# Kernel optimization log

Hardware: AMD Instinct MI355X
Metric: run time of the kernel (lower is better)

## Reference

```python
import jax, jax.numpy as jnp
import numpy as np

EPS = 1e-5


def gcn_conv(x, W, b, src, dst, ew, num_nodes):
    """GCNConv with add_self_loops=True, symmetric normalization (PyG default)."""
    # degree at destination, self-loop weight 1.0 included implicitly
    deg = jax.ops.segment_sum(ew, dst, num_segments=num_nodes) + 1.0  # [N]
    dinv = jax.lax.rsqrt(deg)                                         # deg >= 1
    norm = dinv[src] * ew * dinv[dst]                                 # [E]
    h = x @ W                                                         # [N, F]
    msg = norm[:, None] * h[src]                                      # [E, F]
    agg = jax.ops.segment_sum(msg, dst, num_segments=num_nodes)       # [N, F]
    # self-loop contribution: dinv[i] * 1 * dinv[i] = 1/deg[i]
    agg = agg + h * (1.0 / deg)[:, None]
    return agg + b


def batchnorm(h, gamma, beta):
    mean = jnp.mean(h, axis=0)
    var = jnp.mean(jnp.square(h - mean), axis=0)  # biased, training-mode stats
    return (h - mean) * jax.lax.rsqrt(var + EPS) * gamma + beta


def setup_inputs() -> dict:
    key = jax.random.key(0)
    ks = jax.random.split(key, 8)
    N, E, F = 50000, 800000, 64
    x = jax.random.normal(ks[0], (N, F), dtype=jnp.float32)
    edge_index = jax.random.randint(ks[1], (2, E), 0, N, dtype=jnp.int64)
    edge_weight = jax.random.uniform(ks[2], (E,), dtype=jnp.float32)
    s = 1.0 / np.sqrt(F)
    W1 = jax.random.uniform(ks[3], (F, F), jnp.float32, -s, s)
    b1 = jnp.zeros((F,), jnp.float32)
    W2 = jax.random.uniform(ks[4], (F, F), jnp.float32, -s, s)
    b2 = jnp.zeros((F,), jnp.float32)
    gamma1 = jnp.ones((F,), jnp.float32)
    beta1 = jnp.zeros((F,), jnp.float32)
    gamma2 = jnp.ones((F,), jnp.float32)
    beta2 = jnp.zeros((F,), jnp.float32)
    return {"x": x, "edge_index": edge_index, "edge_weight": edge_weight,
            "W1": W1, "b1": b1, "gamma1": gamma1, "beta1": beta1,
            "W2": W2, "b2": b2, "gamma2": gamma2, "beta2": beta2}


def reference(x, edge_index, edge_weight, W1, b1, gamma1, beta1, W2, b2, gamma2, beta2):
    N = x.shape[0]
    src, dst = edge_index[0], edge_index[1]
    identity = x
    out = gcn_conv(x, W1, b1, src, dst, edge_weight, N)
    out = jax.nn.relu(batchnorm(out, gamma1, beta1))
    out = gcn_conv(out, W2, b2, src, dst, edge_weight, N)
    out = batchnorm(out, gamma2, beta2)
    out = out + identity  # residual: num_input_features == hidden_dim
    return jax.nn.relu(out)
```

## Files before the change

### kernel.cpp

```cpp
#include <hip/hip_runtime.h>
#include <math.h>

#define FEAT 64
#define BN_EPS 1e-5f
#define BN_REPS 64

__device__ __forceinline__ int edge_idx(const void* p, int is64, long long i) {
    return is64 ? (int)((const long long*)p)[i] : ((const int*)p)[i];
}

__device__ __forceinline__ float4 f4fma(float a, float4 b, float4 c) {
    return make_float4(fmaf(a, b.x, c.x), fmaf(a, b.y, c.y),
                       fmaf(a, b.z, c.z), fmaf(a, b.w, c.w));
}

__device__ __forceinline__ unsigned bf16rtne(float f) {
    unsigned u = __float_as_uint(f);
    return (u + 0x7fffu + ((u >> 16) & 1u)) >> 16;
}
__device__ __forceinline__ unsigned packbf2(float a, float b) {
    return bf16rtne(a) | (bf16rtne(b) << 16);
}
__device__ __forceinline__ float4 unpackbf4(uint2 r) {
    return make_float4(__uint_as_float(r.x << 16),
                       __uint_as_float(r.x & 0xffff0000u),
                       __uint_as_float(r.y << 16),
                       __uint_as_float(r.y & 0xffff0000u));
}

__global__ __launch_bounds__(256) void init_kernel(
    const unsigned* __restrict__ w, int* __restrict__ flag,
    int* __restrict__ cnt, float* __restrict__ parts, int N) {
    int i = blockIdx.x * 256 + threadIdx.x;
    if (i < N) cnt[i] = 0;
    if (blockIdx.x < 64) parts[blockIdx.x * 256 + threadIdx.x] = 0.0f;
    if (blockIdx.x == 0 && threadIdx.x < 64) {
        unsigned long long ok = __ballot(w[2 * threadIdx.x + 1] == 0u);
        if (threadIdx.x == 0) *flag = (ok == ~0ull);
    }
}

__global__ __launch_bounds__(256) void count_seq_kernel(
    const void* __restrict__ ei, const int* __restrict__ flag,
    int* __restrict__ cnt, int* __restrict__ seq, int E) {
    int is64 = *flag;
    int T = gridDim.x * 256;
    int i = blockIdx.x * 256 + threadIdx.x;
#pragma unroll
    for (int u = 0; u < 8; ++u) {
        int e = i + u * T;
        if (e < E) {
            int dst = edge_idx(ei, is64, (long long)E + e);
            seq[e] = atomicAdd(&cnt[dst], 1);
        }
    }
}

__global__ __launch_bounds__(256) void scan1_kernel(const int* __restrict__ cnt,
                                                    int* __restrict__ excl,
                                                    int* __restrict__ bsum, int N) {
    __shared__ int tmp[256];
    int i = blockIdx.x * 256 + threadIdx.x;
    int v = (i < N) ? cnt[i] : 0;
    tmp[threadIdx.x] = v;
    __syncthreads();
    for (int off = 1; off < 256; off <<= 1) {
        int t = (threadIdx.x >= off) ? tmp[threadIdx.x - off] : 0;
        __syncthreads();
        tmp[threadIdx.x] += t;
        __syncthreads();
    }
    if (i < N) excl[i] = tmp[threadIdx.x] - v;
    if (threadIdx.x == 255) bsum[blockIdx.x] = tmp[255];
}

__global__ __launch_bounds__(256) void scan2_kernel(int* __restrict__ bsum, int nb) {
    __shared__ int tmp[256];
    int i = threadIdx.x;
    int v = (i < nb) ? bsum[i] : 0;
    tmp[i] = v;
    __syncthreads();
    for (int off = 1; off < 256; off <<= 1) {
        int t = (i >= off) ? tmp[i - off] : 0;
        __syncthreads();
        tmp[i] += t;
        __syncthreads();
    }
    if (i < nb) bsum[i] = tmp[i] - v;
}

__global__ void scan3_kernel(const int* __restrict__ excl,
                             const int* __restrict__ bsum,
                             int* __restrict__ rowptr, int N, int E) {
    int i = blockIdx.x * 256 + threadIdx.x;
    if (i < N) rowptr[i] = excl[i] + bsum[blockIdx.x];
    if (i == 0) rowptr[N] = E;
}

__global__ __launch_bounds__(256) void scatter_csr_kernel(
    const void* __restrict__ ei, const float* __restrict__ ew,
    const int* __restrict__ flag, const int* __restrict__ rowptr,
    const int* __restrict__ seq, int2* __restrict__ csr, int E) {
    int is64 = *flag;
    int T = gridDim.x * 256;
    int i = blockIdx.x * 256 + threadIdx.x;
#pragma unroll
    for (int u = 0; u < 2; ++u) {
        int e = i + u * T;
        if (e < E) {
            int src = edge_idx(ei, is64, e);
            int dst = edge_idx(ei, is64, (long long)E + e);
            int pos = rowptr[dst] + seq[e];
            csr[pos] = make_int2(src, __float_as_int(ew[e]));
        }
    }
}

__global__ __launch_bounds__(256) void deg_inv_kernel(
    const int* __restrict__ rowptr, const int2* __restrict__ csr,
    float* __restrict__ dinv, float* __restrict__ invdeg, int N) {
    int t = blockIdx.x * 256 + threadIdx.x;
    int n = t >> 3, l = t & 7;
    if (n >= N) return;
    int b = rowptr[n], e = rowptr[n + 1];
    float d = 0.0f;
    for (int k = b + l; k < e; k += 8) d += __int_as_float(csr[k].y);
    d += __shfl_xor(d, 1);
    d += __shfl_xor(d, 2);
    d += __shfl_xor(d, 4);
    if (l == 0) {
        d += 1.0f;
        dinv[n]   = rsqrtf(d);
        invdeg[n] = 1.0f / d;
    }
}

__global__ __launch_bounds__(256) void fold_kernel(int2* __restrict__ csr,
                                                   const float* __restrict__ dinv,
                                                   int E) {
    int T = gridDim.x * 256;
    int i = blockIdx.x * 256 + threadIdx.x;
#pragma unroll
    for (int u = 0; u < 2; ++u) {
        int e = i + u * T;
        if (e < E) {
            int2 v = csr[e];
            csr[e].y = __float_as_int(dinv[v.x] * __int_as_float(v.y));
        }
    }
}

__global__ __launch_bounds__(256) void gemm64_kernel(
    const float* __restrict__ in, const float* __restrict__ W,
    const float* __restrict__ scale, const float* __restrict__ shift,
    uint2* __restrict__ out_bf, int N, int affine) {
    __shared__ float4 Ws4[64][16];
    __shared__ float xs[64][65];
    __shared__ float sA[64], sS[64];
    int tid = threadIdx.x;
    const float4* W4 = (const float4*)W;
    for (int j = tid; j < 1024; j += 256) Ws4[j >> 4][j & 15] = W4[j];
    if (affine && tid < 64) { sA[tid] = scale[tid]; sS[tid] = shift[tid]; }
    __syncthreads();

    int rowBase = blockIdx.x * 64;
    for (int j = tid; j < 1024; j += 256) {
        int r = j >> 4, q = j & 15;
        int row = rowBase + r;
        float4 v = make_float4(0.f, 0.f, 0.f, 0.f);
        if (row < N) {
            v = ((const float4*)in)[(size_t)row * 16 + q];
            if (affine) {
                int c = q * 4;
                v.x = fmaxf(fmaf(v.x, sA[c + 0], sS[c + 0]), 0.f);
                v.y = fmaxf(fmaf(v.y, sA[c + 1], sS[c + 1]), 0.f);
                v.z = fmaxf(fmaf(v.z, sA[c + 2], sS[c + 2]), 0.f);
                v.w = fmaxf(fmaf(v.w, sA[c + 3], sS[c + 3]), 0.f);
            }
        }
        xs[r][q * 4 + 0] = v.x;
        xs[r][q * 4 + 1] = v.y;
        xs[r][q * 4 + 2] = v.z;
        xs[r][q * 4 + 3] = v.w;
    }
    __syncthreads();

    int q = tid & 15, rg = tid >> 4;
    int r0 = rg * 4;
    float4 a0 = make_float4(0.f, 0.f, 0.f, 0.f), a1 = a0, a2 = a0, a3 = a0;
#pragma unroll 4
    for (int k = 0; k < 64; ++k) {
        float4 wv = Ws4[k][q];
        a0 = f4fma(xs[r0 + 0][k], wv, a0);
        a1 = f4fma(xs[r0 + 1][k], wv, a1);
        a2 = f4fma(xs[r0 + 2][k], wv, a2);
        a3 = f4fma(xs[r0 + 3][k], wv, a3);
    }
    int row = rowBase + r0;
    if (row + 0 < N) out_bf[(size_t)(row + 0) * 16 + q] = make_uint2(packbf2(a0.x, a0.y), packbf2(a0.z, a0.w));
    if (row + 1 < N) out_bf[(size_t)(row + 1) * 16 + q] = make_uint2(packbf2(a1.x, a1.y), packbf2(a1.z, a1.w));
    if (row + 2 < N) out_bf[(size_t)(row + 2) * 16 + q] = make_uint2(packbf2(a2.x, a2.y), packbf2(a2.z, a2.w));
    if (row + 3 < N) out_bf[(size_t)(row + 3) * 16 + q] = make_uint2(packbf2(a3.x, a3.y), packbf2(a3.z, a3.w));
}

__global__ __launch_bounds__(256) void gather_agg_kernel(
    const uint2* __restrict__ h2, const int* __restrict__ rowptr,
    const int2* __restrict__ csr, const float* __restrict__ dinv,
    const float* __restrict__ invdeg, const float* __restrict__ bias,
    float* __restrict__ agg, float* __restrict__ parts, int N) {
    int tid = threadIdx.x;
    int wave = tid >> 6, lane = tid & 63;
    int sub = lane >> 4, sl = lane & 15;
    float4 bv = ((const float4*)bias)[sl];
    float4 bnS = make_float4(0.f, 0.f, 0.f, 0.f), bnQ = bnS;

    int n = blockIdx.x * 4 + wave;
    if (n < N) {
        int beg = rowptr[n], end = rowptr[n + 1];
        uint2 selfr = h2[(size_t)n * 16 + sl];
        float dn = dinv[n], idg = invdeg[n];

        float4 accE = make_float4(0.f, 0.f, 0.f, 0.f);
        for (int k = beg; k < end; k += 16) {
            int srcs[4]; float w[4];
#pragma unroll
            for (int j = 0; j < 4; ++j) {
                int idx = k + sub + 4 * j;
                if (idx < end) {
                    int2 ed = csr[idx];
                    srcs[j] = ed.x; w[j] = __int_as_float(ed.y);
                } else { srcs[j] = 0; w[j] = 0.f; }
            }
            uint2 hr[4];
#pragma unroll
            for (int j = 0; j < 4; ++j)
                hr[j] = (k + sub + 4 * j < end)
                          ? h2[(size_t)srcs[j] * 16 + sl] : make_uint2(0u, 0u);
#pragma unroll
            for (int j = 0; j < 4; ++j)
                accE = f4fma(w[j], unpackbf4(hr[j]), accE);
        }
        accE.x += __shfl_xor(accE.x, 16); accE.y += __shfl_xor(accE.y, 16);
        accE.z += __shfl_xor(accE.z, 16); accE.w += __shfl_xor(accE.w, 16);
        accE.x += __shfl_xor(accE.x, 32); accE.y += __shfl_xor(accE.y, 32);
        accE.z += __shfl_xor(accE.z, 32); accE.w += __shfl_xor(accE.w, 32);

        if (sub == 0) {
            float4 self = unpackbf4(selfr);
            float4 tot = f4fma(idg, self, bv);
            tot = f4fma(dn, accE, tot);
            ((float4*)agg)[(size_t)n * 16 + sl] = tot;
            bnS.x += tot.x; bnS.y += tot.y; bnS.z += tot.z; bnS.w += tot.w;
            bnQ.x = fmaf(tot.x, tot.x, bnQ.x); bnQ.y = fmaf(tot.y, tot.y, bnQ.y);
            bnQ.z = fmaf(tot.z, tot.z, bnQ.z); bnQ.w = fmaf(tot.w, tot.w, bnQ.w);
        }
    }

    __shared__ float4 LS[4][16], LQ[4][16];
    if (sub == 0) { LS[wave][sl] = bnS; LQ[wave][sl] = bnQ; }
    __syncthreads();
    if (tid < 16) {
        float4 ts = LS[0][tid], tq = LQ[0][tid];
        for (int i = 1; i < 4; ++i) {
            float4 a = LS[i][tid], b = LQ[i][tid];
            ts.x += a.x; ts.y += a.y; ts.z += a.z; ts.w += a.w;
            tq.x += b.x; tq.y += b.y; tq.z += b.z; tq.w += b.w;
        }
        float* P = parts + (size_t)(blockIdx.x & (BN_REPS - 1)) * 128;
        int c = tid * 4;
        unsafeAtomicAdd(&P[c + 0], ts.x);      unsafeAtomicAdd(&P[c + 1], ts.y);
        unsafeAtomicAdd(&P[c + 2], ts.z);      unsafeAtomicAdd(&P[c + 3], ts.w);
        unsafeAtomicAdd(&P[64 + c + 0], tq.x); unsafeAtomicAdd(&P[64 + c + 1], tq.y);
        unsafeAtomicAdd(&P[64 + c + 2], tq.z); unsafeAtomicAdd(&P[64 + c + 3], tq.w);
    }
}

__global__ void bn_final_kernel(const float* __restrict__ parts,
                                const float* __restrict__ gamma,
                                const float* __restrict__ beta,
                                float* __restrict__ a, float* __restrict__ s,
                                float invN) {
    int c = threadIdx.x;
    if (c < 64) {
        float sm = 0.f, sq = 0.f;
        for (int r = 0; r < BN_REPS; ++r) {
            sm += parts[r * 128 + c];
            sq += parts[r * 128 + 64 + c];
        }
        float m = sm * invN;
        float var = fmaxf(sq * invN - m * m, 0.0f);
        float aa = gamma[c] * rsqrtf(var + BN_EPS);
        a[c] = aa;
        s[c] = beta[c] - m * aa;
    }
}

__global__ void final_out_kernel(const float* __restrict__ agg,
                                 const float* __restrict__ a,
                                 const float* __restrict__ s,
                                 const float* __restrict__ x,
                                 float* __restrict__ out, int nquads) {
    int gid = blockIdx.x * 256 + threadIdx.x;
    if (gid < nquads) {
        int q = gid & 15;
        float4 av = ((const float4*)a)[q], sv = ((const float4*)s)[q];
        float4 g = ((const float4*)agg)[gid], xv = ((const float4*)x)[gid];
        float4 o;
        o.x = fmaxf(fmaf(g.x, av.x, sv.x) + xv.x, 0.f);
        o.y = fmaxf(fmaf(g.y, av.y, sv.y) + xv.y, 0.f);
        o.z = fmaxf(fmaf(g.z, av.z, sv.z) + xv.z, 0.f);
        o.w = fmaxf(fmaf(g.w, av.w, sv.w) + xv.w, 0.f);
        ((float4*)out)[gid] = o;
    }
}

extern "C" void kernel_launch(void* const* d_in, const int* in_sizes, int n_in,
                              void* d_out, int out_size, void* d_ws, size_t ws_size,
                              hipStream_t stream) {
    const float* x      = (const float*)d_in[0];
    const void*  ei     = d_in[1];
    const float* ew     = (const float*)d_in[2];
    const float* W1     = (const float*)d_in[3];
    const float* b1     = (const float*)d_in[4];
    const float* gamma1 = (const float*)d_in[5];
    const float* beta1  = (const float*)d_in[6];
    const float* W2     = (const float*)d_in[7];
    const float* b2     = (const float*)d_in[8];
    const float* gamma2 = (const float*)d_in[9];
    const float* beta2  = (const float*)d_in[10];
    float* out = (float*)d_out;

    const int N = in_sizes[0] / FEAT;
    const int E = in_sizes[2];

    char* ws = (char*)d_ws;
    size_t off = 0;
    auto alloc = [&](size_t bytes) {
        size_t o = off;
        off += (bytes + 255) & ~(size_t)255;
        return (void*)(ws + o);
    };
    int*   flag   = (int*)  alloc(256);
    int*   cnt    = (int*)  alloc((size_t)N * 4);
    int*   rowptr = (int*)  alloc((size_t)(N + 1) * 4);
    int*   seq    = (int*)  alloc((size_t)E * 4);
    int*   excl   = (int*)  alloc((size_t)N * 4);
    int*   bsum   = (int*)  alloc(256 * 4);
    float* dinv   = (float*)alloc((size_t)N * 4);
    float* invdeg = (float*)alloc((size_t)N * 4);
    float* parts  = (float*)alloc(2 * BN_REPS * 128 * 4);
    float* ab     = (float*)alloc(256 * 4);
    int2*  csr    = (int2*) alloc((size_t)E * 8);
    uint2* h_bf   = (uint2*)alloc((size_t)N * 16 * 8);
    float* agg    = (float*)alloc((size_t)N * FEAT * 4);

    const int nblkN  = (N + 255) / 256;
    const int nblkN8 = (N * 8 + 255) / 256;
    const int nblkE8 = (E + 2047) / 2048;
    const int nblkE2 = (E + 511) / 512;
    const int nblkQ  = (N * 16 + 255) / 256;
    const int nblkG  = (N + 63) / 64;
    const int nblkA  = (N + 3) / 4;

    init_kernel<<<nblkN, 256, 0, stream>>>((const unsigned*)ei, flag, cnt, parts, N);
    count_seq_kernel<<<nblkE8, 256, 0, stream>>>(ei, flag, cnt, seq, E);
    scan1_kernel<<<nblkN, 256, 0, stream>>>(cnt, excl, bsum, N);
    scan2_kernel<<<1, 256, 0, stream>>>(bsum, nblkN);
    scan3_kernel<<<nblkN, 256, 0, stream>>>(excl, bsum, rowptr, N, E);
    scatter_csr_kernel<<<nblkE2, 256, 0, stream>>>(ei, ew, flag, rowptr, seq, csr, E);
    deg_inv_kernel<<<nblkN8, 256, 0, stream>>>(rowptr, csr, dinv, invdeg, N);
    fold_kernel<<<nblkE2, 256, 0, stream>>>(csr, dinv, E);

    gemm64_kernel<<<nblkG, 256, 0, stream>>>(x, W1, nullptr, nullptr, h_bf, N, 0);
    gather_agg_kernel<<<nblkA, 256, 0, stream>>>(h_bf, rowptr, csr, dinv,
                                                 invdeg, b1, agg, parts, N);
    bn_final_kernel<<<1, 64, 0, stream>>>(parts, gamma1, beta1,
                                          ab, ab + 64, 1.0f / (float)N);

    gemm64_kernel<<<nblkG, 256, 0, stream>>>(agg, W2, ab, ab + 64, h_bf, N, 1);
    gather_agg_kernel<<<nblkA, 256, 0, stream>>>(h_bf, rowptr, csr, dinv,
                                                 invdeg, b2, agg,
                                                 parts + BN_REPS * 128, N);
    bn_final_kernel<<<1, 64, 0, stream>>>(parts + BN_REPS * 128, gamma2, beta2,
                                          ab + 128, ab + 192, 1.0f / (float)N);

    final_out_kernel<<<nblkQ, 256, 0, stream>>>(agg, ab + 128, ab + 192, x,
                                                out, N * 16);
}
```

Baseline: 208.6 us.

## Split bf16 features into two half-planes and gather each half separately

The GEMM now writes its bf16 output as two column-half planes (32 features each) instead of interleaved rows. The gather kernel launches twice as many blocks, each handling one feature half with 8 lanes per edge and 8 edges in flight per wave. The goal is a smaller per-half working set for the random-access feature gathers, for better cache hit rate. CSR loads also become nontemporal. The cost is that the CSR index stream is read twice and there are twice as many blocks and BN atomics.

```diff
diff --git a/kernel.cpp b/kernel.cpp
--- a/kernel.cpp
+++ b/kernel.cpp
@@ -163,6 +163,7 @@
     if (affine && tid < 64) { sA[tid] = scale[tid]; sS[tid] = shift[tid]; }
     __syncthreads();
 
+    size_t pstride = (size_t)N * 8;
     int rowBase = blockIdx.x * 64;
     for (int j = tid; j < 1024; j += 256) {
         int r = j >> 4, q = j & 15;
@@ -197,10 +198,11 @@
         a3 = f4fma(xs[r0 + 3][k], wv, a3);
     }
     int row = rowBase + r0;
-    if (row + 0 < N) out_bf[(size_t)(row + 0) * 16 + q] = make_uint2(packbf2(a0.x, a0.y), packbf2(a0.z, a0.w));
-    if (row + 1 < N) out_bf[(size_t)(row + 1) * 16 + q] = make_uint2(packbf2(a1.x, a1.y), packbf2(a1.z, a1.w));
-    if (row + 2 < N) out_bf[(size_t)(row + 2) * 16 + q] = make_uint2(packbf2(a2.x, a2.y), packbf2(a2.z, a2.w));
-    if (row + 3 < N) out_bf[(size_t)(row + 3) * 16 + q] = make_uint2(packbf2(a3.x, a3.y), packbf2(a3.z, a3.w));
+    size_t base = (size_t)(q >> 3) * pstride + (q & 7);
+    if (row + 0 < N) out_bf[base + (size_t)(row + 0) * 8] = make_uint2(packbf2(a0.x, a0.y), packbf2(a0.z, a0.w));
+    if (row + 1 < N) out_bf[base + (size_t)(row + 1) * 8] = make_uint2(packbf2(a1.x, a1.y), packbf2(a1.z, a1.w));
+    if (row + 2 < N) out_bf[base + (size_t)(row + 2) * 8] = make_uint2(packbf2(a2.x, a2.y), packbf2(a2.z, a2.w));
+    if (row + 3 < N) out_bf[base + (size_t)(row + 3) * 8] = make_uint2(packbf2(a3.x, a3.y), packbf2(a3.z, a3.w));
 }
 
 __global__ __launch_bounds__(256) void gather_agg_kernel(
@@ -210,36 +212,42 @@
     float* __restrict__ agg, float* __restrict__ parts, int N) {
     int tid = threadIdx.x;
     int wave = tid >> 6, lane = tid & 63;
-    int sub = lane >> 4, sl = lane & 15;
-    float4 bv = ((const float4*)bias)[sl];
+    int sub = lane >> 3, sl = lane & 7;
+    int half = blockIdx.x & 1;
+    int n = (blockIdx.x >> 1) * 4 + wave;
+    const uint2* hp = h2 + (size_t)half * (size_t)N * 8;
+    float4 bv = ((const float4*)bias)[half * 8 + sl];
     float4 bnS = make_float4(0.f, 0.f, 0.f, 0.f), bnQ = bnS;
 
-    int n = blockIdx.x * 4 + wave;
     if (n < N) {
         int beg = rowptr[n], end = rowptr[n + 1];
-        uint2 selfr = h2[(size_t)n * 16 + sl];
+        uint2 selfr = hp[(size_t)n * 8 + sl];
         float dn = dinv[n], idg = invdeg[n];
 
         float4 accE = make_float4(0.f, 0.f, 0.f, 0.f);
-        for (int k = beg; k < end; k += 16) {
+        for (int k = beg; k < end; k += 32) {
             int srcs[4]; float w[4];
 #pragma unroll
             for (int j = 0; j < 4; ++j) {
-                int idx = k + sub + 4 * j;
+                int idx = k + sub + 8 * j;
                 if (idx < end) {
-                    int2 ed = csr[idx];
-                    srcs[j] = ed.x; w[j] = __int_as_float(ed.y);
+                    unsigned long long v = __builtin_nontemporal_load(
+                        (const unsigned long long*)&csr[idx]);
+                    srcs[j] = (int)(v & 0xffffffffull);
+                    w[j] = __uint_as_float((unsigned)(v >> 32));
                 } else { srcs[j] = 0; w[j] = 0.f; }
             }
             uint2 hr[4];
 #pragma unroll
             for (int j = 0; j < 4; ++j)
-                hr[j] = (k + sub + 4 * j < end)
-                          ? h2[(size_t)srcs[j] * 16 + sl] : make_uint2(0u, 0u);
+                hr[j] = (k + sub + 8 * j < end)
+                          ? hp[(size_t)srcs[j] * 8 + sl] : make_uint2(0u, 0u);
 #pragma unroll
             for (int j = 0; j < 4; ++j)
                 accE = f4fma(w[j], unpackbf4(hr[j]), accE);
         }
+        accE.x += __shfl_xor(accE.x, 8);  accE.y += __shfl_xor(accE.y, 8);
+        accE.z += __shfl_xor(accE.z, 8);  accE.w += __shfl_xor(accE.w, 8);
         accE.x += __shfl_xor(accE.x, 16); accE.y += __shfl_xor(accE.y, 16);
         accE.z += __shfl_xor(accE.z, 16); accE.w += __shfl_xor(accE.w, 16);
         accE.x += __shfl_xor(accE.x, 32); accE.y += __shfl_xor(accE.y, 32);
@@ -249,25 +257,25 @@
             float4 self = unpackbf4(selfr);
             float4 tot = f4fma(idg, self, bv);
             tot = f4fma(dn, accE, tot);
-            ((float4*)agg)[(size_t)n * 16 + sl] = tot;
+            ((float4*)agg)[(size_t)n * 16 + half * 8 + sl] = tot;
             bnS.x += tot.x; bnS.y += tot.y; bnS.z += tot.z; bnS.w += tot.w;
             bnQ.x = fmaf(tot.x, tot.x, bnQ.x); bnQ.y = fmaf(tot.y, tot.y, bnQ.y);
             bnQ.z = fmaf(tot.z, tot.z, bnQ.z); bnQ.w = fmaf(tot.w, tot.w, bnQ.w);
         }
     }
 
-    __shared__ float4 LS[4][16], LQ[4][16];
+    __shared__ float4 LS[4][8], LQ[4][8];
     if (sub == 0) { LS[wave][sl] = bnS; LQ[wave][sl] = bnQ; }
     __syncthreads();
-    if (tid < 16) {
+    if (tid < 8) {
         float4 ts = LS[0][tid], tq = LQ[0][tid];
         for (int i = 1; i < 4; ++i) {
             float4 a = LS[i][tid], b = LQ[i][tid];
             ts.x += a.x; ts.y += a.y; ts.z += a.z; ts.w += a.w;
             tq.x += b.x; tq.y += b.y; tq.z += b.z; tq.w += b.w;
         }
-        float* P = parts + (size_t)(blockIdx.x & (BN_REPS - 1)) * 128;
-        int c = tid * 4;
+        float* P = parts + (size_t)((blockIdx.x >> 1) & (BN_REPS - 1)) * 128;
+        int c = half * 32 + tid * 4;
         unsafeAtomicAdd(&P[c + 0], ts.x);      unsafeAtomicAdd(&P[c + 1], ts.y);
         unsafeAtomicAdd(&P[c + 2], ts.z);      unsafeAtomicAdd(&P[c + 3], ts.w);
         unsafeAtomicAdd(&P[64 + c + 0], tq.x); unsafeAtomicAdd(&P[64 + c + 1], tq.y);
@@ -360,7 +368,7 @@
     const int nblkE2 = (E + 511) / 512;
     const int nblkQ  = (N * 16 + 255) / 256;
     const int nblkG  = (N + 63) / 64;
-    const int nblkA  = (N + 3) / 4;
+    const int nblkA  = 2 * ((N + 3) / 4);
 
     init_kernel<<<nblkN, 256, 0, stream>>>((const unsigned*)ei, flag, cnt, parts, N);
     count_seq_kernel<<<nblkE8, 256, 0, stream>>>(ei, flag, cnt, seq, E);
```

New measurement: 216.0 us. 3.5% more time.
